# Kernel tuning notes

Measured on AMD Instinct MI355X. Metric: run time of the kernel, lower is better.

## Reference

```python
import jax, jax.numpy as jnp
import numpy as np

B = 64        # graphs
N0 = 2048     # nodes per graph
DEG = 16      # avg degree
IN = 128      # input_dim
H = 30        # hcs
NH = 11       # heads
OD = 8        # output_dim[i]
K1, K2, K3 = 1844, 1660, 1494  # ceil(0.9*n) chain


def setup_inputs() -> dict:
    key = jax.random.key(0)
    ks = jax.random.split(key, 32)
    N = B * N0
    E = N * DEG
    x = jax.random.normal(ks[0], (N, IN), jnp.float32)
    g = jnp.repeat(jnp.arange(B, dtype=jnp.int32), N0 * DEG)
    src = g * N0 + jax.random.randint(ks[1], (E,), 0, N0, dtype=jnp.int32)
    dst = g * N0 + jax.random.randint(ks[2], (E,), 0, N0, dtype=jnp.int32)
    edge_index = jnp.stack([src, dst])
    edge_attr = jax.random.uniform(ks[3], (E,), jnp.float32)
    batch = jnp.repeat(jnp.arange(B, dtype=jnp.int32), N0)
    s = 0.05
    def W(k, *shape):
        return jax.random.normal(k, shape, jnp.float32) * s
    return {
        'x': x, 'edge_index': edge_index, 'edge_attr': edge_attr, 'batch': batch,
        'ln_g': jnp.ones((IN,), jnp.float32), 'ln_b': jnp.zeros((IN,), jnp.float32),
        'W_rel1': W(ks[4], IN, H), 'b_rel1': W(ks[5], H), 'W_root1': W(ks[6], IN, H),
        'W_rel2': W(ks[7], H, H), 'b_rel2': W(ks[8], H), 'W_root2': W(ks[9], H, H),
        'W_rel3': W(ks[10], H, H), 'b_rel3': W(ks[11], H), 'W_root3': W(ks[12], H, H),
        'pool_w1': W(ks[13], H), 'pool_w2': W(ks[14], H), 'pool_w3': W(ks[15], H),
        'head_W1': W(ks[16], NH, 2 * H, 8 * H), 'head_b1': W(ks[17], NH, 8 * H),
        'head_W2': W(ks[18], NH, 8 * H, 32 * H), 'head_b2': W(ks[19], NH, 32 * H),
        'head_W3': W(ks[20], NH, 32 * H, OD), 'head_b3': W(ks[21], NH, OD),
    }


def _layernorm(x, g, b):
    m = x.mean(-1, keepdims=True)
    v = ((x - m) ** 2).mean(-1, keepdims=True)
    return (x - m) * jax.lax.rsqrt(v + 1e-5) * g + b


def _gconv(x, src, dst, ew, Wr, br, Ws, N):
    # PyG GraphConv: out = lin_rel(sum_j ew*x_j) + lin_root(x)
    agg = jax.ops.segment_sum(x[src] * ew[:, None], dst, num_segments=N)
    return agg @ Wr + br + x @ Ws


def _topk_pool(x, src, dst, ew, w, n, k):
    # score = tanh(x.w/||w||); keep top-k per graph; gate kept nodes by score
    score = jnp.tanh((x @ w) / jnp.linalg.norm(w)).reshape(B, n)
    vals, idx = jax.lax.top_k(score, k)                      # [B,k]
    xg = x.reshape(B, n, -1)
    xk = jnp.take_along_axis(xg, idx[:, :, None], axis=1) * vals[:, :, None]
    x_new = xk.reshape(B * k, -1)
    newidx = jnp.full((B, n), -1, jnp.int32)
    newidx = newidx.at[jnp.arange(B)[:, None], idx].set(
        jnp.broadcast_to(jnp.arange(k, dtype=jnp.int32), (B, k)))
    g = src // n
    ns = newidx[g, src % n]
    nd = newidx[g, dst % n]
    keep = (ns >= 0) & (nd >= 0)
    src_new = jnp.where(keep, g * k + ns, 0)
    dst_new = jnp.where(keep, g * k + nd, 0)
    ew_new = jnp.where(keep, ew, 0.0)
    return x_new, src_new, dst_new, ew_new


def _readout(x, k):
    xg = x.reshape(B, k, -1)
    return jnp.concatenate([xg.max(axis=1), xg.mean(axis=1)], axis=1)  # [B,2H]


def reference(x, edge_index, edge_attr, batch, ln_g, ln_b,
              W_rel1, b_rel1, W_root1, W_rel2, b_rel2, W_root2,
              W_rel3, b_rel3, W_root3, pool_w1, pool_w2, pool_w3,
              head_W1, head_b1, head_W2, head_b2, head_W3, head_b3):
    src, dst = edge_index[0], edge_index[1]
    ew = edge_attr
    h = _layernorm(x, ln_g, ln_b)

    h = jax.nn.relu(_gconv(h, src, dst, ew, W_rel1, b_rel1, W_root1, B * N0))
    h, src, dst, ew = _topk_pool(h, src, dst, ew, pool_w1, N0, K1)
    x1 = _readout(h, K1)

    h = jax.nn.relu(_gconv(h, src, dst, ew, W_rel2, b_rel2, W_root2, B * K1))
    h, src, dst, ew = _topk_pool(h, src, dst, ew, pool_w2, K1, K2)
    x2 = _readout(h, K2)

    h = jax.nn.relu(_gconv(h, src, dst, ew, W_rel3, b_rel3, W_root3, B * K2))
    h, src, dst, ew = _topk_pool(h, src, dst, ew, pool_w3, K2, K3)
    x3 = _readout(h, K3)

    z = jax.nn.relu(x1 + x2 + x3)                                   # [B,60]
    a = jax.nn.relu(jnp.einsum('bd,hdo->hbo', z, head_W1) + head_b1[:, None, :])
    a = jax.nn.relu(jnp.einsum('hbo,hop->hbp', a, head_W2) + head_b2[:, None, :])
    out = jnp.einsum('hbp,hpq->hbq', a, head_W3) + head_b3[:, None, :]
    return out  # [11, B, 8]
```

## Files before the change

kernel.cpp:

```cpp
#include <hip/hip_runtime.h>
#include <hip/hip_bf16.h>

#define B 64
#define N0 2048
#define DEG 16
#define IN_DIM 128
#define H 30
#define NH 11
#define K1 1844
#define K2 1660
#define K3 1494
#define NTOT (B * N0)
#define ETOT (NTOT * DEG)
#define EPG (ETOT / B)
#define RSTRIDE 32
#define ESTRIDE1 32768
#define ESTRIDE2 27648
#define RSEG 16

__global__ __launch_bounds__(256) void k_prep(
    const float* __restrict__ ln_g, const float* __restrict__ ln_b,
    const float* __restrict__ Wrel1, const float* __restrict__ brel1, const float* __restrict__ Wroot1,
    const float* __restrict__ Wrel2, const float* __restrict__ Wroot2,
    const float* __restrict__ Wrel3, const float* __restrict__ Wroot3,
    float* __restrict__ Wc1, float* __restrict__ S1, float* __restrict__ T1,
    float* __restrict__ Wc2, float* __restrict__ Wc3)
{
    int tid = threadIdx.x;
    for (int i = tid; i < IN_DIM * 60; i += 256) {
        int j = i / 60, c = i - j * 60;
        float w = (c < H) ? Wrel1[j * H + c] : Wroot1[j * H + (c - H)];
        Wc1[i] = w * ln_g[j];
    }
    if (tid < 60) {
        int c = tid;
        float s = 0.f, tt = 0.f;
        for (int j = 0; j < IN_DIM; ++j) {
            float w = (c < H) ? Wrel1[j * H + c] : Wroot1[j * H + (c - H)];
            s += w * ln_g[j];
            tt += w * ln_b[j];
        }
        S1[c] = s;
        T1[c] = (c < H) ? tt : tt + brel1[c - H];
    }
    for (int i = tid; i < H * 60; i += 256) {
        int j = i / 60, c = i - j * 60;
        Wc2[i] = (c < H) ? Wrel2[j * H + c] : Wroot2[j * H + (c - H)];
        Wc3[i] = (c < H) ? Wrel3[j * H + c] : Wroot3[j * H + (c - H)];
    }
}

__global__ __launch_bounds__(256) void k_lnproj(
    const float* __restrict__ x, const float* __restrict__ Wc,
    const float* __restrict__ S, const float* __restrict__ T,
    float* __restrict__ r, float* __restrict__ t)
{
    int row = blockIdx.x * 256 + threadIdx.x;
    const float* xr = x + (size_t)row * IN_DIM;
    float acc[60];
#pragma unroll
    for (int c = 0; c < 60; ++c) acc[c] = 0.f;
    float sum = 0.f, sumsq = 0.f;
    for (int jb = 0; jb < IN_DIM; jb += 8) {
        float4 a0 = *(const float4*)(xr + jb);
        float4 a1 = *(const float4*)(xr + jb + 4);
        float xs[8] = {a0.x, a0.y, a0.z, a0.w, a1.x, a1.y, a1.z, a1.w};
#pragma unroll
        for (int u = 0; u < 8; ++u) {
            float xv = xs[u];
            sum += xv;
            sumsq += xv * xv;
            const float* wrow = Wc + (jb + u) * 60;
#pragma unroll
            for (int c = 0; c < 60; ++c) acc[c] += xv * wrow[c];
        }
    }
    float mean = sum * (1.f / 128.f);
    float var = sumsq * (1.f / 128.f) - mean * mean;
    float rstd = 1.0f / sqrtf(var + 1e-5f);
    int rb = row * RSTRIDE, tb = row * H;
#pragma unroll
    for (int c = 0; c < H; ++c)
        r[rb + c] = rstd * (acc[c] - mean * S[c]) + T[c];
#pragma unroll
    for (int c = 0; c < H; ++c)
        t[tb + c] = rstd * (acc[30 + c] - mean * S[30 + c]) + T[30 + c];
}

__global__ __launch_bounds__(256) void k_proj30p(
    const float* __restrict__ hbuf, const int* __restrict__ sidx,
    const float* __restrict__ score, const float* __restrict__ Wc,
    const float* __restrict__ brel, float* __restrict__ r, float* __restrict__ t,
    int n_old, int k)
{
    int row = blockIdx.x * 256 + threadIdx.x;
    int g = row / k, j = row - g * k;
    int idx = sidx[g * k + j];
    float val = score[g * n_old + idx];
    const float* hr = hbuf + (size_t)(g * n_old + idx) * RSTRIDE;
    float hv[32];
#pragma unroll
    for (int m = 0; m < 8; ++m) {
        float4 q = *(const float4*)(hr + m * 4);
        hv[m * 4] = q.x; hv[m * 4 + 1] = q.y; hv[m * 4 + 2] = q.z; hv[m * 4 + 3] = q.w;
    }
    float acc[60];
#pragma unroll
    for (int c = 0; c < 60; ++c) acc[c] = 0.f;
    for (int m = 0; m < H; ++m) {
        const float* wrow = Wc + m * 60;
        float xv = hv[m];
#pragma unroll
        for (int c = 0; c < 60; ++c) acc[c] += xv * wrow[c];
    }
    int rb = row * RSTRIDE, tb = row * H;
#pragma unroll
    for (int c = 0; c < H; ++c) r[rb + c] = val * acc[c];
#pragma unroll
    for (int c = 0; c < H; ++c) t[tb + c] = val * acc[30 + c] + brel[c];
}

__global__ __launch_bounds__(1024) void k_hist1(
    const int* __restrict__ dst, unsigned short* __restrict__ rank,
    int* __restrict__ chunkCnt)
{
    __shared__ unsigned int cnt[2048];
    int chunk = blockIdx.x, g = chunk >> 2;
    for (int i = threadIdx.x; i < 2048; i += 1024) cnt[i] = 0;
    __syncthreads();
    int e0 = chunk * 8192;
#pragma unroll
    for (int u = 0; u < 8; ++u) {
        int e = e0 + u * 1024 + threadIdx.x;
        int d = dst[e] - g * N0;
        rank[e] = (unsigned short)atomicAdd(&cnt[d], 1u);
    }
    __syncthreads();
    for (int i = threadIdx.x; i < 2048; i += 1024) chunkCnt[chunk * 2048 + i] = cnt[i];
}

__global__ __launch_bounds__(1024) void k_scat1(
    const int* __restrict__ src, const int* __restrict__ dst, const float* __restrict__ ew,
    const unsigned short* __restrict__ rank, const int* __restrict__ chunkOff,
    float2* __restrict__ sOut)
{
    int chunk = blockIdx.x, g = chunk >> 2;
    int e0 = chunk * 8192;
#pragma unroll
    for (int u = 0; u < 8; ++u) {
        int e = e0 + u * 1024 + threadIdx.x;
        int d = dst[e] - g * N0;
        int pos = chunkOff[chunk * 2048 + d] + (int)rank[e];
        sOut[(size_t)g * ESTRIDE1 + pos] = make_float2(__int_as_float(src[e]), ew[e]);
    }
}

__global__ __launch_bounds__(1024) void k_histE(
    const int* __restrict__ src0, const int* __restrict__ dst0,
    const int* __restrict__ mapc, unsigned short* __restrict__ rank,
    int* __restrict__ chunkCnt)
{
    __shared__ unsigned int cnt[2048];
    int chunk = blockIdx.x;
    for (int i = threadIdx.x; i < 2048; i += 1024) cnt[i] = 0;
    __syncthreads();
    int e0 = chunk * 8192;
#pragma unroll
    for (int u = 0; u < 8; ++u) {
        int e = e0 + u * 1024 + threadIdx.x;
        int dd = mapc[dst0[e]];
        int ss = mapc[src0[e]];
        if (dd >= 0 && ss >= 0)
            rank[e] = (unsigned short)atomicAdd(&cnt[dd], 1u);
    }
    __syncthreads();
    for (int i = threadIdx.x; i < 2048; i += 1024) chunkCnt[chunk * 2048 + i] = cnt[i];
}

__global__ __launch_bounds__(1024) void k_scatE(
    const int* __restrict__ src0, const int* __restrict__ dst0,
    const float* __restrict__ ew, const int* __restrict__ mapc,
    const unsigned short* __restrict__ rank, const int* __restrict__ chunkOff,
    float2* __restrict__ sOut, int k_new, int estride)
{
    int chunk = blockIdx.x, g = chunk >> 2;
    int e0 = chunk * 8192;
#pragma unroll
    for (int u = 0; u < 8; ++u) {
        int e = e0 + u * 1024 + threadIdx.x;
        int dd = mapc[dst0[e]];
        int ss = mapc[src0[e]];
        if (dd >= 0 && ss >= 0) {
            int pos = chunkOff[chunk * 2048 + dd] + (int)rank[e];
            sOut[(size_t)g * estride + pos] =
                make_float2(__int_as_float(g * k_new + ss), ew[e]);
        }
    }
}

__global__ __launch_bounds__(1024) void k_scan(
    int* __restrict__ chunkCnt, int* __restrict__ runStart, int* __restrict__ runLen)
{
    __shared__ int bufA[2048], bufB[2048];
    int g = blockIdx.x;
    int c0[2], c1[2], c2[2], tt[2];
    for (int h2 = 0; h2 < 2; ++h2) {
        int d = threadIdx.x + h2 * 1024;
        c0[h2] = chunkCnt[(g * 4 + 0) * 2048 + d];
        c1[h2] = chunkCnt[(g * 4 + 1) * 2048 + d];
        c2[h2] = chunkCnt[(g * 4 + 2) * 2048 + d];
        int c3 = chunkCnt[(g * 4 + 3) * 2048 + d];
        tt[h2] = c0[h2] + c1[h2] + c2[h2] + c3;
        bufA[d] = tt[h2];
    }
    __syncthreads();
    int* s_ = bufA; int* d_ = bufB;
    for (int off = 1; off < 2048; off <<= 1) {
        for (int h2 = 0; h2 < 2; ++h2) {
            int d = threadIdx.x + h2 * 1024;
            int v = s_[d];
            if (d >= off) v += s_[d - off];
            d_[d] = v;
        }
        __syncthreads();
        int* tmp = s_; s_ = d_; d_ = tmp;
    }
    for (int h2 = 0; h2 < 2; ++h2) {
        int d = threadIdx.x + h2 * 1024;
        int ex = s_[d] - tt[h2];
        runStart[g * 2048 + d] = ex;
        runLen[g * 2048 + d] = tt[h2];
        chunkCnt[(g * 4 + 0) * 2048 + d] = ex;
        chunkCnt[(g * 4 + 1) * 2048 + d] = ex + c0[h2];
        chunkCnt[(g * 4 + 2) * 2048 + d] = ex + c0[h2] + c1[h2];
        chunkCnt[(g * 4 + 3) * 2048 + d] = ex + c0[h2] + c1[h2] + c2[h2];
    }
}

__global__ __launch_bounds__(256) void k_gather(
    const float2* __restrict__ sE, const int* __restrict__ runS, const int* __restrict__ runL,
    const float* __restrict__ rp, const float* __restrict__ t, float* __restrict__ h,
    const float* __restrict__ poolw, float* __restrict__ score,
    int n, int estride, int nblocks)
{
    int b = blockIdx.x;
    int cpx = nblocks >> 3;
    b = (b & 7) * cpx + (b >> 3);
    int slot = threadIdx.x >> 5, j = threadIdx.x & 31;
    int v = b * 8 + slot;
    int g = v / n;
    int local = v - g * n;
    int s0 = runS[g * 2048 + local], len = runL[g * 2048 + local];
    const float2* meta = sE + (size_t)g * estride + s0;
    float acc = 0.f;
    for (int c = 0; c < len; c += 8) {
        int lim = len - c; if (lim > 8) lim = 8;
        float2 m[8];
#pragma unroll
        for (int u = 0; u < 8; ++u) m[u] = meta[c + (u < lim ? u : 0)];
#pragma unroll
        for (int u = 0; u < 8; ++u) {
            int s = __float_as_int(m[u].x);
            float w = (u < lim) ? m[u].y : 0.f;
            acc += rp[(size_t)s * RSTRIDE + j] * w;
        }
    }
    float wj = (j < H) ? poolw[j] : 0.f;
    float hval = 0.f;
    if (j < H) {
        hval = fmaxf(acc + t[v * H + j], 0.f);
        h[(size_t)v * RSTRIDE + j] = hval;
    }
    float p = hval * wj, q = wj * wj;
#pragma unroll
    for (int off = 16; off > 0; off >>= 1) {
        p += __shfl_xor(p, off, 32);
        q += __shfl_xor(q, off, 32);
    }
    if (j == 0) score[v] = tanhf(p / sqrtf(q));
}

__global__ __launch_bounds__(1024) void k_topk_map(
    const float* __restrict__ score, int* __restrict__ sidx, int* __restrict__ mapc,
    int n, int k, int first)
{
    __shared__ unsigned long long keys[2048];
    __shared__ int inv[2048];
    int g = blockIdx.x;
    for (int i = threadIdx.x; i < 2048; i += 1024) {
        unsigned long long key = ~0ull;
        if (i < n) {
            float s = score[g * n + i];
            if (s == 0.f) s = 0.f;
            unsigned u = __float_as_uint(s);
            unsigned asc = (u & 0x80000000u) ? ~u : (u | 0x80000000u);
            unsigned desc = ~asc;
            key = ((unsigned long long)desc << 32) | (unsigned)i;
        }
        keys[i] = key;
        inv[i] = -1;
    }
    __syncthreads();
    for (int kk = 2; kk <= 2048; kk <<= 1) {
        for (int jj = kk >> 1; jj > 0; jj >>= 1) {
            for (int i = threadIdx.x; i < 2048; i += 1024) {
                int ixj = i ^ jj;
                if (ixj > i) {
                    unsigned long long a = keys[i], bb = keys[ixj];
                    bool up = ((i & kk) == 0);
                    if ((a > bb) == up) { keys[i] = bb; keys[ixj] = a; }
                }
            }
            __syncthreads();
        }
    }
    for (int j = threadIdx.x; j < k; j += 1024) {
        int idx = (int)(keys[j] & 0xffffffffu);
        sidx[g * k + j] = idx;
        inv[idx] = j;
    }
    __syncthreads();
    if (first) {
        for (int v = threadIdx.x; v < N0; v += 1024)
            mapc[g * N0 + v] = inv[v];
    } else {
        for (int v = threadIdx.x; v < N0; v += 1024) {
            int m = mapc[g * N0 + v];
            mapc[g * N0 + v] = (m >= 0) ? inv[m] : -1;
        }
    }
}

__global__ __launch_bounds__(256) void k_rpart(
    const float* __restrict__ hbuf, const int* __restrict__ sidx,
    const float* __restrict__ score, float* __restrict__ pmax, float* __restrict__ psum,
    int n_old, int k)
{
    __shared__ float smax[8][32], ssum[8][32];
    int g = blockIdx.y, seg = blockIdx.x;
    int clen = (k + RSEG - 1) / RSEG;
    int start = seg * clen;
    int end = start + clen; if (end > k) end = k;
    int f = threadIdx.x & 31, rr = threadIdx.x >> 5;
    float mx = -INFINITY, sm = 0.f;
    if (f < H) {
        for (int j = start + rr; j < end; j += 8) {
            int idx = sidx[g * k + j];
            float val = score[g * n_old + idx];
            float v = hbuf[(size_t)(g * n_old + idx) * RSTRIDE + f] * val;
            mx = fmaxf(mx, v);
            sm += v;
        }
    }
    smax[rr][f] = mx; ssum[rr][f] = sm;
    __syncthreads();
    if (rr == 0) {
        for (int q = 1; q < 8; ++q) { mx = fmaxf(mx, smax[q][f]); sm += ssum[q][f]; }
        pmax[(g * RSEG + seg) * 32 + f] = mx;
        psum[(g * RSEG + seg) * 32 + f] = sm;
    }
}

__global__ __launch_bounds__(64) void k_zfin(
    const float* __restrict__ pm1, const float* __restrict__ ps1,
    const float* __restrict__ pm2, const float* __restrict__ ps2,
    const float* __restrict__ pm3, const float* __restrict__ ps3,
    float* __restrict__ z)
{
    int g = blockIdx.x, c = threadIdx.x;
    if (c >= 60) return;
    float v1, v2, v3;
    if (c < H) {
        float m1 = -INFINITY, m2 = -INFINITY, m3 = -INFINITY;
        for (int s = 0; s < RSEG; ++s) {
            m1 = fmaxf(m1, pm1[(g * RSEG + s) * 32 + c]);
            m2 = fmaxf(m2, pm2[(g * RSEG + s) * 32 + c]);
            m3 = fmaxf(m3, pm3[(g * RSEG + s) * 32 + c]);
        }
        v1 = m1; v2 = m2; v3 = m3;
    } else {
        int f = c - H;
        float s1 = 0.f, s2 = 0.f, s3 = 0.f;
        for (int s = 0; s < RSEG; ++s) {
            s1 += ps1[(g * RSEG + s) * 32 + f];
            s2 += ps2[(g * RSEG + s) * 32 + f];
            s3 += ps3[(g * RSEG + s) * 32 + f];
        }
        v1 = s1 / (float)K1; v2 = s2 / (float)K2; v3 = s3 / (float)K3;
    }
    z[g * 60 + c] = fmaxf(v1 + v2 + v3, 0.f);
}

__global__ __launch_bounds__(256) void k_mlp1(
    const float* __restrict__ z, const float* __restrict__ W,
    const float* __restrict__ bias, float* __restrict__ a)
{
    int hb = blockIdx.x, hh = hb >> 6, b = hb & 63;
    __shared__ float zr[60];
    if (threadIdx.x < 60) zr[threadIdx.x] = z[b * 60 + threadIdx.x];
    __syncthreads();
    int o = threadIdx.x;
    if (o < 240) {
        float acc = bias[hh * 240 + o];
        const float* Wp = W + hh * 60 * 240;
#pragma unroll
        for (int d = 0; d < 60; ++d) acc += zr[d] * Wp[d * 240 + o];
        a[(hh * B + b) * 240 + o] = fmaxf(acc, 0.f);
    }
}

__global__ __launch_bounds__(320) void k_mlp2(
    const float* __restrict__ a1, const float* __restrict__ W,
    const float* __restrict__ bias, float* __restrict__ a2)
{
    int hh = blockIdx.x >> 3;
    int bb = (blockIdx.x & 7) * 8;
    __shared__ float ar[8][240];
    for (int i = threadIdx.x; i < 8 * 240; i += 320) {
        int rr = i / 240, o = i - rr * 240;
        ar[rr][o] = a1[(hh * B + bb + rr) * 240 + o];
    }
    __syncthreads();
    const float* Wp = W + hh * 240 * 960;
    float accv[3][8];
#pragma unroll
    for (int q = 0; q < 3; ++q)
#pragma unroll
        for (int rr = 0; rr < 8; ++rr) accv[q][rr] = 0.f;
#pragma unroll 2
    for (int o = 0; o < 240; ++o) {
        float w0 = Wp[o * 960 + threadIdx.x];
        float w1 = Wp[o * 960 + threadIdx.x + 320];
        float w2 = Wp[o * 960 + threadIdx.x + 640];
#pragma unroll
        for (int rr = 0; rr < 8; ++rr) {
            float av = ar[rr][o];
            accv[0][rr] += w0 * av;
            accv[1][rr] += w1 * av;
            accv[2][rr] += w2 * av;
        }
    }
#pragma unroll
    for (int q = 0; q < 3; ++q) {
        int p = threadIdx.x + q * 320;
        float bv = bias[hh * 960 + p];
#pragma unroll
        for (int rr = 0; rr < 8; ++rr)
            a2[(hh * B + bb + rr) * 960 + p] = fmaxf(accv[q][rr] + bv, 0.f);
    }
}

__global__ __launch_bounds__(64) void k_mlp3(
    const float* __restrict__ a2, const float* __restrict__ W,
    const float* __restrict__ bias, float* __restrict__ out)
{
    int hb = blockIdx.x, hh = hb >> 6, b = hb & 63;
    __shared__ float ar[960];
    __shared__ float part[64];
    for (int i = threadIdx.x; i < 960; i += 64) ar[i] = a2[(hh * B + b) * 960 + i];
    __syncthreads();
    int q = threadIdx.x & 7, c = threadIdx.x >> 3;
    const float* Wp = W + hh * 960 * 8;
    float acc = 0.f;
    for (int p = c; p < 960; p += 8) acc += ar[p] * Wp[p * 8 + q];
    part[threadIdx.x] = acc;
    __syncthreads();
    if (threadIdx.x < 8) {
        float s = bias[hh * 8 + threadIdx.x];
        for (int cc = 0; cc < 8; ++cc) s += part[cc * 8 + threadIdx.x];
        out[(hh * B + b) * 8 + threadIdx.x] = s;
    }
}

extern "C" void kernel_launch(void* const* d_in, const int* in_sizes, int n_in,
                              void* d_out, int out_size, void* d_ws, size_t ws_size,
                              hipStream_t stream)
{
    const float* x       = (const float*)d_in[0];
    const int*   eidx    = (const int*)d_in[1];
    const int*   src0    = eidx;
    const int*   dst0    = eidx + ETOT;
    const float* ew0     = (const float*)d_in[2];
    const float* ln_g    = (const float*)d_in[4];
    const float* ln_b    = (const float*)d_in[5];
    const float* W_rel1  = (const float*)d_in[6];
    const float* b_rel1  = (const float*)d_in[7];
    const float* W_root1 = (const float*)d_in[8];
    const float* W_rel2  = (const float*)d_in[9];
    const float* b_rel2  = (const float*)d_in[10];
    const float* W_root2 = (const float*)d_in[11];
    const float* W_rel3  = (const float*)d_in[12];
    const float* b_rel3  = (const float*)d_in[13];
    const float* W_root3 = (const float*)d_in[14];
    const float* pool_w1 = (const float*)d_in[15];
    const float* pool_w2 = (const float*)d_in[16];
    const float* pool_w3 = (const float*)d_in[17];
    const float* head_W1 = (const float*)d_in[18];
    const float* head_b1 = (const float*)d_in[19];
    const float* head_W2 = (const float*)d_in[20];
    const float* head_b2 = (const float*)d_in[21];
    const float* head_W3 = (const float*)d_in[22];
    const float* head_b3 = (const float*)d_in[23];

    float* ws     = (float*)d_ws;
    float* rbuf   = ws;
    float* tbuf   = rbuf + (size_t)NTOT * RSTRIDE;
    float* abuf   = tbuf + (size_t)NTOT * H;
    float2* sA    = (float2*)(abuf + (size_t)NTOT * RSTRIDE);
    float2* sB    = sA + (size_t)B * ESTRIDE1;
    float* score  = (float*)(sB + (size_t)B * ESTRIDE2);
    int*   sidx   = (int*)(score + NTOT);
    int*   mapc   = sidx + NTOT;
    int*   runSA  = mapc + NTOT;
    int*   runLA  = runSA + B * 2048;
    int*   runSB  = runLA + B * 2048;
    int*   runLB  = runSB + B * 2048;
    float* pm1    = (float*)(runLB + B * 2048);
    float* ps1    = pm1 + B * RSEG * 32;
    float* pm2    = ps1 + B * RSEG * 32;
    float* ps2    = pm2 + B * RSEG * 32;
    float* pm3    = ps2 + B * RSEG * 32;
    float* ps3    = pm3 + B * RSEG * 32;
    float* zb     = ps3 + B * RSEG * 32;
    float* Wc1    = zb + B * 60;
    float* S1     = Wc1 + IN_DIM * 60;
    float* T1     = S1 + 60;
    float* Wc2    = T1 + 60;
    float* Wc3    = Wc2 + H * 60;
    int* chunkBuf         = (int*)abuf;
    unsigned short* rank  = (unsigned short*)((char*)abuf + (4u << 20));
    float* a1 = rbuf;
    float* a2 = a1 + NH * B * 240;

    k_prep<<<1, 256, 0, stream>>>(ln_g, ln_b, W_rel1, b_rel1, W_root1,
                                  W_rel2, W_root2, W_rel3, W_root3,
                                  Wc1, S1, T1, Wc2, Wc3);

    k_hist1<<<256, 1024, 0, stream>>>(dst0, rank, chunkBuf);
    k_scan<<<B, 1024, 0, stream>>>(chunkBuf, runSA, runLA);
    k_scat1<<<256, 1024, 0, stream>>>(src0, dst0, ew0, rank, chunkBuf, sA);
    k_lnproj<<<NTOT / 256, 256, 0, stream>>>(x, Wc1, S1, T1, rbuf, tbuf);
    k_gather<<<NTOT / 8, 256, 0, stream>>>(sA, runSA, runLA, rbuf, tbuf, abuf,
                                           pool_w1, score, N0, ESTRIDE1, NTOT / 8);
    k_topk_map<<<B, 1024, 0, stream>>>(score, sidx, mapc, N0, K1, 1);
    k_rpart<<<dim3(RSEG, B), 256, 0, stream>>>(abuf, sidx, score, pm1, ps1, N0, K1);
    k_proj30p<<<B * K1 / 256, 256, 0, stream>>>(abuf, sidx, score, Wc2, b_rel2,
                                                rbuf, tbuf, N0, K1);

    k_histE<<<256, 1024, 0, stream>>>(src0, dst0, mapc, rank, chunkBuf);
    k_scan<<<B, 1024, 0, stream>>>(chunkBuf, runSB, runLB);
    k_scatE<<<256, 1024, 0, stream>>>(src0, dst0, ew0, mapc, rank, chunkBuf, sB,
                                      K1, ESTRIDE2);
    k_gather<<<B * K1 / 8, 256, 0, stream>>>(sB, runSB, runLB, rbuf, tbuf, abuf,
                                             pool_w2, score, K1, ESTRIDE2, B * K1 / 8);
    k_topk_map<<<B, 1024, 0, stream>>>(score, sidx, mapc, K1, K2, 0);
    k_rpart<<<dim3(RSEG, B), 256, 0, stream>>>(abuf, sidx, score, pm2, ps2, K1, K2);
    k_proj30p<<<B * K2 / 256, 256, 0, stream>>>(abuf, sidx, score, Wc3, b_rel3,
                                                rbuf, tbuf, K1, K2);

    k_histE<<<256, 1024, 0, stream>>>(src0, dst0, mapc, rank, chunkBuf);
    k_scan<<<B, 1024, 0, stream>>>(chunkBuf, runSA, runLA);
    k_scatE<<<256, 1024, 0, stream>>>(src0, dst0, ew0, mapc, rank, chunkBuf, sA,
                                      K2, ESTRIDE1);
    k_gather<<<B * K2 / 8, 256, 0, stream>>>(sA, runSA, runLA, rbuf, tbuf, abuf,
                                             pool_w3, score, K2, ESTRIDE1, B * K2 / 8);
    k_topk_map<<<B, 1024, 0, stream>>>(score, sidx, mapc, K2, K3, 0);
    k_rpart<<<dim3(RSEG, B), 256, 0, stream>>>(abuf, sidx, score, pm3, ps3, K2, K3);

    k_zfin<<<B, 64, 0, stream>>>(pm1, ps1, pm2, ps2, pm3, ps3, zb);
    k_mlp1<<<NH * B, 256, 0, stream>>>(zb, head_W1, head_b1, a1);
    k_mlp2<<<NH * 8, 320, 0, stream>>>(a1, head_W2, head_b2, a2);
    k_mlp3<<<NH * B, 64, 0, stream>>>(a2, head_W3, head_b3, (float*)d_out);
}
```

Before: 577.2 us.

## Reuse level-0 CSR with index remap, retile projections and head MLP

```diff
diff --git a/kernel.cpp b/kernel.cpp
--- a/kernel.cpp
+++ b/kernel.cpp
@@ -15,7 +15,6 @@
 #define EPG (ETOT / B)
 #define RSTRIDE 32
 #define ESTRIDE1 32768
-#define ESTRIDE2 27648
 #define RSEG 16
 
 __global__ __launch_bounds__(256) void k_prep(
@@ -55,36 +54,82 @@
     const float* __restrict__ S, const float* __restrict__ T,
     float* __restrict__ r, float* __restrict__ t)
 {
-    int row = blockIdx.x * 256 + threadIdx.x;
-    const float* xr = x + (size_t)row * IN_DIM;
-    float acc[60];
-#pragma unroll
-    for (int c = 0; c < 60; ++c) acc[c] = 0.f;
-    float sum = 0.f, sumsq = 0.f;
-    for (int jb = 0; jb < IN_DIM; jb += 8) {
-        float4 a0 = *(const float4*)(xr + jb);
-        float4 a1 = *(const float4*)(xr + jb + 4);
-        float xs[8] = {a0.x, a0.y, a0.z, a0.w, a1.x, a1.y, a1.z, a1.w};
-#pragma unroll
-        for (int u = 0; u < 8; ++u) {
-            float xv = xs[u];
-            sum += xv;
-            sumsq += xv * xv;
-            const float* wrow = Wc + (jb + u) * 60;
-#pragma unroll
-            for (int c = 0; c < 60; ++c) acc[c] += xv * wrow[c];
-        }
-    }
-    float mean = sum * (1.f / 128.f);
-    float var = sumsq * (1.f / 128.f) - mean * mean;
-    float rstd = 1.0f / sqrtf(var + 1e-5f);
-    int rb = row * RSTRIDE, tb = row * H;
-#pragma unroll
-    for (int c = 0; c < H; ++c)
-        r[rb + c] = rstd * (acc[c] - mean * S[c]) + T[c];
-#pragma unroll
-    for (int c = 0; c < H; ++c)
-        t[tb + c] = rstd * (acc[30 + c] - mean * S[30 + c]) + T[30 + c];
+    __shared__ float wlds[4][IN_DIM][16];
+    for (int i = threadIdx.x; i < IN_DIM * 64; i += 256) {
+        int k = i >> 6, cc = i & 63;
+        int cg = cc >> 4, j = cc & 15;
+        wlds[cg][k][j] = (j < 15) ? Wc[k * 60 + cg * 15 + j] : 0.f;
+    }
+    __syncthreads();
+    int lane = threadIdx.x & 63, cg = threadIdx.x >> 6;
+    int row0 = blockIdx.x * 512 + lane;
+    const float* xb = x + (size_t)row0 * IN_DIM;
+    float acc[8][15];
+    float sum[8], sumsq[8];
+#pragma unroll
+    for (int ri = 0; ri < 8; ++ri) {
+        sum[ri] = 0.f; sumsq[ri] = 0.f;
+#pragma unroll
+        for (int c = 0; c < 15; ++c) acc[ri][c] = 0.f;
+    }
+    float4 cur[8], nxt[8];
+#pragma unroll
+    for (int ri = 0; ri < 8; ++ri)
+        cur[ri] = *(const float4*)(xb + (size_t)ri * 64 * IN_DIM);
+    for (int kb = 0; kb < 32; ++kb) {
+        if (kb < 31) {
+#pragma unroll
+            for (int ri = 0; ri < 8; ++ri)
+                nxt[ri] = *(const float4*)(xb + (size_t)ri * 64 * IN_DIM + (kb + 1) * 4);
+        }
+#pragma unroll
+        for (int kk = 0; kk < 4; ++kk) {
+            int k = kb * 4 + kk;
+            float4 w0 = *(const float4*)&wlds[cg][k][0];
+            float4 w1 = *(const float4*)&wlds[cg][k][4];
+            float4 w2 = *(const float4*)&wlds[cg][k][8];
+            float4 w3 = *(const float4*)&wlds[cg][k][12];
+#pragma unroll
+            for (int ri = 0; ri < 8; ++ri) {
+                float xv = (kk == 0) ? cur[ri].x : (kk == 1) ? cur[ri].y
+                          : (kk == 2) ? cur[ri].z : cur[ri].w;
+                sum[ri] += xv; sumsq[ri] += xv * xv;
+                acc[ri][0]  += xv * w0.x; acc[ri][1]  += xv * w0.y;
+                acc[ri][2]  += xv * w0.z; acc[ri][3]  += xv * w0.w;
+                acc[ri][4]  += xv * w1.x; acc[ri][5]  += xv * w1.y;
+                acc[ri][6]  += xv * w1.z; acc[ri][7]  += xv * w1.w;
+                acc[ri][8]  += xv * w2.x; acc[ri][9]  += xv * w2.y;
+                acc[ri][10] += xv * w2.z; acc[ri][11] += xv * w2.w;
+                acc[ri][12] += xv * w3.x; acc[ri][13] += xv * w3.y;
+                acc[ri][14] += xv * w3.z;
+            }
+        }
+        if (kb < 31) {
+#pragma unroll
+            for (int ri = 0; ri < 8; ++ri) cur[ri] = nxt[ri];
+        }
+    }
+    bool isR = (cg < 2);
+    int cbase = (cg & 1) * 15;
+    float* outp = isR ? r : t;
+    float sS[15], sT[15];
+#pragma unroll
+    for (int c = 0; c < 15; ++c) { sS[c] = S[cg * 15 + c]; sT[c] = T[cg * 15 + c]; }
+#pragma unroll
+    for (int ri = 0; ri < 8; ++ri) {
+        int row = row0 + ri * 64;
+        float mean = sum[ri] * (1.f / 128.f);
+        float var = sumsq[ri] * (1.f / 128.f) - mean * mean;
+        float rstd = 1.0f / sqrtf(var + 1e-5f);
+        float* op = outp + (size_t)row * RSTRIDE + cbase;
+#pragma unroll
+        for (int c = 0; c < 15; ++c)
+            op[c] = rstd * (acc[ri][c] - mean * sS[c]) + sT[c];
+        if (cg & 1) {
+            outp[(size_t)row * RSTRIDE + 30] = 0.f;
+            outp[(size_t)row * RSTRIDE + 31] = 0.f;
+        }
+    }
 }
 
 __global__ __launch_bounds__(256) void k_proj30p(
@@ -93,31 +138,100 @@
     const float* __restrict__ brel, float* __restrict__ r, float* __restrict__ t,
     int n_old, int k)
 {
-    int row = blockIdx.x * 256 + threadIdx.x;
-    int g = row / k, j = row - g * k;
-    int idx = sidx[g * k + j];
-    float val = score[g * n_old + idx];
-    const float* hr = hbuf + (size_t)(g * n_old + idx) * RSTRIDE;
-    float hv[32];
-#pragma unroll
-    for (int m = 0; m < 8; ++m) {
-        float4 q = *(const float4*)(hr + m * 4);
-        hv[m * 4] = q.x; hv[m * 4 + 1] = q.y; hv[m * 4 + 2] = q.z; hv[m * 4 + 3] = q.w;
-    }
-    float acc[60];
-#pragma unroll
-    for (int c = 0; c < 60; ++c) acc[c] = 0.f;
-    for (int m = 0; m < H; ++m) {
-        const float* wrow = Wc + m * 60;
-        float xv = hv[m];
-#pragma unroll
-        for (int c = 0; c < 60; ++c) acc[c] += xv * wrow[c];
-    }
-    int rb = row * RSTRIDE, tb = row * H;
-#pragma unroll
-    for (int c = 0; c < H; ++c) r[rb + c] = val * acc[c];
-#pragma unroll
-    for (int c = 0; c < H; ++c) t[tb + c] = val * acc[30 + c] + brel[c];
+    __shared__ float wlds[4][32][16];
+    for (int i = threadIdx.x; i < 30 * 64; i += 256) {
+        int m = i >> 6, cc = i & 63;
+        int cg = cc >> 4, j = cc & 15;
+        wlds[cg][m][j] = (j < 15) ? Wc[m * 60 + cg * 15 + j] : 0.f;
+    }
+    __syncthreads();
+    int lane = threadIdx.x & 63, cg = threadIdx.x >> 6;
+    int row0 = blockIdx.x * 256 + lane;
+    float acc[4][15];
+#pragma unroll
+    for (int ri = 0; ri < 4; ++ri)
+#pragma unroll
+        for (int c = 0; c < 15; ++c) acc[ri][c] = 0.f;
+    float vals[4];
+    const float* hp[4];
+#pragma unroll
+    for (int ri = 0; ri < 4; ++ri) {
+        int row = row0 + ri * 64;
+        int g = row / k, j = row - g * k;
+        int idx = sidx[g * k + j];
+        vals[ri] = score[g * n_old + idx];
+        hp[ri] = hbuf + (size_t)(g * n_old + idx) * RSTRIDE;
+    }
+    for (int mb = 0; mb < 7; ++mb) {
+        float4 cur[4];
+#pragma unroll
+        for (int ri = 0; ri < 4; ++ri) cur[ri] = *(const float4*)(hp[ri] + mb * 4);
+#pragma unroll
+        for (int kk = 0; kk < 4; ++kk) {
+            int m = mb * 4 + kk;
+            float4 w0 = *(const float4*)&wlds[cg][m][0];
+            float4 w1 = *(const float4*)&wlds[cg][m][4];
+            float4 w2 = *(const float4*)&wlds[cg][m][8];
+            float4 w3 = *(const float4*)&wlds[cg][m][12];
+#pragma unroll
+            for (int ri = 0; ri < 4; ++ri) {
+                float xv = (kk == 0) ? cur[ri].x : (kk == 1) ? cur[ri].y
+                          : (kk == 2) ? cur[ri].z : cur[ri].w;
+                acc[ri][0]  += xv * w0.x; acc[ri][1]  += xv * w0.y;
+                acc[ri][2]  += xv * w0.z; acc[ri][3]  += xv * w0.w;
+                acc[ri][4]  += xv * w1.x; acc[ri][5]  += xv * w1.y;
+                acc[ri][6]  += xv * w1.z; acc[ri][7]  += xv * w1.w;
+                acc[ri][8]  += xv * w2.x; acc[ri][9]  += xv * w2.y;
+                acc[ri][10] += xv * w2.z; acc[ri][11] += xv * w2.w;
+                acc[ri][12] += xv * w3.x; acc[ri][13] += xv * w3.y;
+                acc[ri][14] += xv * w3.z;
+            }
+        }
+    }
+    {
+        float2 h2[4];
+#pragma unroll
+        for (int ri = 0; ri < 4; ++ri) h2[ri] = *(const float2*)(hp[ri] + 28);
+#pragma unroll
+        for (int kk = 0; kk < 2; ++kk) {
+            int m = 28 + kk;
+            float4 w0 = *(const float4*)&wlds[cg][m][0];
+            float4 w1 = *(const float4*)&wlds[cg][m][4];
+            float4 w2 = *(const float4*)&wlds[cg][m][8];
+            float4 w3 = *(const float4*)&wlds[cg][m][12];
+#pragma unroll
+            for (int ri = 0; ri < 4; ++ri) {
+                float xv = (kk == 0) ? h2[ri].x : h2[ri].y;
+                acc[ri][0]  += xv * w0.x; acc[ri][1]  += xv * w0.y;
+                acc[ri][2]  += xv * w0.z; acc[ri][3]  += xv * w0.w;
+                acc[ri][4]  += xv * w1.x; acc[ri][5]  += xv * w1.y;
+                acc[ri][6]  += xv * w1.z; acc[ri][7]  += xv * w1.w;
+                acc[ri][8]  += xv * w2.x; acc[ri][9]  += xv * w2.y;
+                acc[ri][10] += xv * w2.z; acc[ri][11] += xv * w2.w;
+                acc[ri][12] += xv * w3.x; acc[ri][13] += xv * w3.y;
+                acc[ri][14] += xv * w3.z;
+            }
+        }
+    }
+    bool isR = (cg < 2);
+    int cbase = (cg & 1) * 15;
+    float* outp = isR ? r : t;
+    float sB[15];
+#pragma unroll
+    for (int c = 0; c < 15; ++c) sB[c] = isR ? 0.f : brel[cbase + c];
+#pragma unroll
+    for (int ri = 0; ri < 4; ++ri) {
+        int row = row0 + ri * 64;
+        float val = vals[ri];
+        float* op = outp + (size_t)row * RSTRIDE + cbase;
+#pragma unroll
+        for (int c = 0; c < 15; ++c)
+            op[c] = val * acc[ri][c] + sB[c];
+        if (cg & 1) {
+            outp[(size_t)row * RSTRIDE + 30] = 0.f;
+            outp[(size_t)row * RSTRIDE + 31] = 0.f;
+        }
+    }
 }
 
 __global__ __launch_bounds__(1024) void k_hist1(
@@ -137,65 +251,6 @@
     }
     __syncthreads();
     for (int i = threadIdx.x; i < 2048; i += 1024) chunkCnt[chunk * 2048 + i] = cnt[i];
-}
-
-__global__ __launch_bounds__(1024) void k_scat1(
-    const int* __restrict__ src, const int* __restrict__ dst, const float* __restrict__ ew,
-    const unsigned short* __restrict__ rank, const int* __restrict__ chunkOff,
-    float2* __restrict__ sOut)
-{
-    int chunk = blockIdx.x, g = chunk >> 2;
-    int e0 = chunk * 8192;
-#pragma unroll
-    for (int u = 0; u < 8; ++u) {
-        int e = e0 + u * 1024 + threadIdx.x;
-        int d = dst[e] - g * N0;
-        int pos = chunkOff[chunk * 2048 + d] + (int)rank[e];
-        sOut[(size_t)g * ESTRIDE1 + pos] = make_float2(__int_as_float(src[e]), ew[e]);
-    }
-}
-
-__global__ __launch_bounds__(1024) void k_histE(
-    const int* __restrict__ src0, const int* __restrict__ dst0,
-    const int* __restrict__ mapc, unsigned short* __restrict__ rank,
-    int* __restrict__ chunkCnt)
-{
-    __shared__ unsigned int cnt[2048];
-    int chunk = blockIdx.x;
-    for (int i = threadIdx.x; i < 2048; i += 1024) cnt[i] = 0;
-    __syncthreads();
-    int e0 = chunk * 8192;
-#pragma unroll
-    for (int u = 0; u < 8; ++u) {
-        int e = e0 + u * 1024 + threadIdx.x;
-        int dd = mapc[dst0[e]];
-        int ss = mapc[src0[e]];
-        if (dd >= 0 && ss >= 0)
-            rank[e] = (unsigned short)atomicAdd(&cnt[dd], 1u);
-    }
-    __syncthreads();
-    for (int i = threadIdx.x; i < 2048; i += 1024) chunkCnt[chunk * 2048 + i] = cnt[i];
-}
-
-__global__ __launch_bounds__(1024) void k_scatE(
-    const int* __restrict__ src0, const int* __restrict__ dst0,
-    const float* __restrict__ ew, const int* __restrict__ mapc,
-    const unsigned short* __restrict__ rank, const int* __restrict__ chunkOff,
-    float2* __restrict__ sOut, int k_new, int estride)
-{
-    int chunk = blockIdx.x, g = chunk >> 2;
-    int e0 = chunk * 8192;
-#pragma unroll
-    for (int u = 0; u < 8; ++u) {
-        int e = e0 + u * 1024 + threadIdx.x;
-        int dd = mapc[dst0[e]];
-        int ss = mapc[src0[e]];
-        if (dd >= 0 && ss >= 0) {
-            int pos = chunkOff[chunk * 2048 + dd] + (int)rank[e];
-            sOut[(size_t)g * estride + pos] =
-                make_float2(__int_as_float(g * k_new + ss), ew[e]);
-        }
-    }
 }
 
 __global__ __launch_bounds__(1024) void k_scan(
@@ -237,11 +292,29 @@
     }
 }
 
+__global__ __launch_bounds__(1024) void k_scat1(
+    const int* __restrict__ src, const int* __restrict__ dst, const float* __restrict__ ew,
+    const unsigned short* __restrict__ rank, const int* __restrict__ chunkOff,
+    float2* __restrict__ sOut)
+{
+    int chunk = blockIdx.x, g = chunk >> 2;
+    int e0 = chunk * 8192;
+#pragma unroll
+    for (int u = 0; u < 8; ++u) {
+        int e = e0 + u * 1024 + threadIdx.x;
+        int d = dst[e] - g * N0;
+        int pos = chunkOff[chunk * 2048 + d] + (int)rank[e];
+        sOut[(size_t)g * ESTRIDE1 + pos] = make_float2(__int_as_float(src[e]), ew[e]);
+    }
+}
+
+template<int LVL>
 __global__ __launch_bounds__(256) void k_gather(
     const float2* __restrict__ sE, const int* __restrict__ runS, const int* __restrict__ runL,
+    const int* __restrict__ ind1, const int* __restrict__ ind2, const int* __restrict__ mapc,
     const float* __restrict__ rp, const float* __restrict__ t, float* __restrict__ h,
     const float* __restrict__ poolw, float* __restrict__ score,
-    int n, int estride, int nblocks)
+    int n, int rK, int nblocks)
 {
     int b = blockIdx.x;
     int cpx = nblocks >> 3;
@@ -250,25 +323,40 @@
     int v = b * 8 + slot;
     int g = v / n;
     int local = v - g * n;
-    int s0 = runS[g * 2048 + local], len = runL[g * 2048 + local];
-    const float2* meta = sE + (size_t)g * estride + s0;
+    int v1 = local;
+    if (LVL >= 2) v1 = ind2[g * K2 + v1];
+    if (LVL >= 1) v1 = ind1[g * K1 + v1];
+    int s0 = runS[g * 2048 + v1], len = runL[g * 2048 + v1];
+    const float2* meta = sE + (size_t)g * ESTRIDE1 + s0;
+    int rbase = g * rK;
     float acc = 0.f;
     for (int c = 0; c < len; c += 8) {
         int lim = len - c; if (lim > 8) lim = 8;
         float2 m[8];
 #pragma unroll
         for (int u = 0; u < 8; ++u) m[u] = meta[c + (u < lim ? u : 0)];
+        int rowv[8]; float wv[8];
 #pragma unroll
         for (int u = 0; u < 8; ++u) {
-            int s = __float_as_int(m[u].x);
+            int srcg = __float_as_int(m[u].x);
             float w = (u < lim) ? m[u].y : 0.f;
-            acc += rp[(size_t)s * RSTRIDE + j] * w;
-        }
+            if (LVL == 0) {
+                rowv[u] = srcg;
+            } else {
+                int ss = mapc[srcg];
+                rowv[u] = rbase + (ss < 0 ? 0 : ss);
+                w = (ss < 0) ? 0.f : w;
+            }
+            wv[u] = w;
+        }
+#pragma unroll
+        for (int u = 0; u < 8; ++u)
+            acc += rp[(size_t)rowv[u] * RSTRIDE + j] * wv[u];
     }
     float wj = (j < H) ? poolw[j] : 0.f;
     float hval = 0.f;
     if (j < H) {
-        hval = fmaxf(acc + t[v * H + j], 0.f);
+        hval = fmaxf(acc + t[(size_t)v * RSTRIDE + j], 0.f);
         h[(size_t)v * RSTRIDE + j] = hval;
     }
     float p = hval * wj, q = wj * wj;
@@ -409,45 +497,34 @@
     }
 }
 
-__global__ __launch_bounds__(320) void k_mlp2(
+__global__ __launch_bounds__(256) void k_mlp2(
     const float* __restrict__ a1, const float* __restrict__ W,
     const float* __restrict__ bias, float* __restrict__ a2)
 {
-    int hh = blockIdx.x >> 3;
-    int bb = (blockIdx.x & 7) * 8;
-    __shared__ float ar[8][240];
-    for (int i = threadIdx.x; i < 8 * 240; i += 320) {
-        int rr = i / 240, o = i - rr * 240;
-        ar[rr][o] = a1[(hh * B + bb + rr) * 240 + o];
-    }
-    __syncthreads();
-    const float* Wp = W + hh * 240 * 960;
-    float accv[3][8];
-#pragma unroll
-    for (int q = 0; q < 3; ++q)
-#pragma unroll
-        for (int rr = 0; rr < 8; ++rr) accv[q][rr] = 0.f;
-#pragma unroll 2
+    __shared__ float a1t[64 * 240];
+    int hh = blockIdx.x / 15, ct = blockIdx.x % 15;
+    const float4* ag = (const float4*)(a1 + (size_t)hh * B * 240);
+    for (int i = threadIdx.x; i < 64 * 240 / 4; i += 256)
+        ((float4*)a1t)[i] = ag[i];
+    __syncthreads();
+    int col = threadIdx.x & 63, rg = threadIdx.x >> 6;
+    const float* Wp = W + (size_t)hh * 240 * 960 + ct * 64 + col;
+    float acc[16];
+#pragma unroll
+    for (int i = 0; i < 16; ++i) acc[i] = 0.f;
+#pragma unroll 4
     for (int o = 0; o < 240; ++o) {
-        float w0 = Wp[o * 960 + threadIdx.x];
-        float w1 = Wp[o * 960 + threadIdx.x + 320];
-        float w2 = Wp[o * 960 + threadIdx.x + 640];
-#pragma unroll
-        for (int rr = 0; rr < 8; ++rr) {
-            float av = ar[rr][o];
-            accv[0][rr] += w0 * av;
-            accv[1][rr] += w1 * av;
-            accv[2][rr] += w2 * av;
-        }
-    }
-#pragma unroll
-    for (int q = 0; q < 3; ++q) {
-        int p = threadIdx.x + q * 320;
-        float bv = bias[hh * 960 + p];
-#pragma unroll
-        for (int rr = 0; rr < 8; ++rr)
-            a2[(hh * B + bb + rr) * 960 + p] = fmaxf(accv[q][rr] + bv, 0.f);
-    }
+        float w = Wp[(size_t)o * 960];
+        const float* ar = &a1t[0];
+#pragma unroll
+        for (int i = 0; i < 16; ++i)
+            acc[i] += w * ar[(rg * 16 + i) * 240 + o];
+    }
+    float bv = bias[hh * 960 + ct * 64 + col];
+#pragma unroll
+    for (int i = 0; i < 16; ++i)
+        a2[((size_t)hh * B + rg * 16 + i) * 960 + ct * 64 + col] =
+            fmaxf(acc[i] + bv, 0.f);
 }
 
 __global__ __launch_bounds__(64) void k_mlp3(
@@ -505,17 +582,16 @@
     float* ws     = (float*)d_ws;
     float* rbuf   = ws;
     float* tbuf   = rbuf + (size_t)NTOT * RSTRIDE;
-    float* abuf   = tbuf + (size_t)NTOT * H;
+    float* abuf   = tbuf + (size_t)NTOT * RSTRIDE;
     float2* sA    = (float2*)(abuf + (size_t)NTOT * RSTRIDE);
-    float2* sB    = sA + (size_t)B * ESTRIDE1;
-    float* score  = (float*)(sB + (size_t)B * ESTRIDE2);
-    int*   sidx   = (int*)(score + NTOT);
-    int*   mapc   = sidx + NTOT;
+    float* score  = (float*)(sA + (size_t)B * ESTRIDE1);
+    int*   sidxA  = (int*)(score + NTOT);
+    int*   sidxB  = sidxA + B * K1;
+    int*   sidxC  = sidxB + B * K2;
+    int*   mapc   = sidxC + B * K3;
     int*   runSA  = mapc + NTOT;
     int*   runLA  = runSA + B * 2048;
-    int*   runSB  = runLA + B * 2048;
-    int*   runLB  = runSB + B * 2048;
-    float* pm1    = (float*)(runLB + B * 2048);
+    float* pm1    = (float*)(runLA + B * 2048);
     float* ps1    = pm1 + B * RSEG * 32;
     float* pm2    = ps1 + B * RSEG * 32;
     float* ps2    = pm2 + B * RSEG * 32;
@@ -539,36 +615,32 @@
     k_hist1<<<256, 1024, 0, stream>>>(dst0, rank, chunkBuf);
     k_scan<<<B, 1024, 0, stream>>>(chunkBuf, runSA, runLA);
     k_scat1<<<256, 1024, 0, stream>>>(src0, dst0, ew0, rank, chunkBuf, sA);
-    k_lnproj<<<NTOT / 256, 256, 0, stream>>>(x, Wc1, S1, T1, rbuf, tbuf);
-    k_gather<<<NTOT / 8, 256, 0, stream>>>(sA, runSA, runLA, rbuf, tbuf, abuf,
-                                           pool_w1, score, N0, ESTRIDE1, NTOT / 8);
-    k_topk_map<<<B, 1024, 0, stream>>>(score, sidx, mapc, N0, K1, 1);
-    k_rpart<<<dim3(RSEG, B), 256, 0, stream>>>(abuf, sidx, score, pm1, ps1, N0, K1);
-    k_proj30p<<<B * K1 / 256, 256, 0, stream>>>(abuf, sidx, score, Wc2, b_rel2,
+
+    k_lnproj<<<NTOT / 512, 256, 0, stream>>>(x, Wc1, S1, T1, rbuf, tbuf);
+    k_gather<0><<<NTOT / 8, 256, 0, stream>>>(sA, runSA, runLA, nullptr, nullptr, nullptr,
+                                              rbuf, tbuf, abuf, pool_w1, score,
+                                              N0, N0, NTOT / 8);
+    k_topk_map<<<B, 1024, 0, stream>>>(score, sidxA, mapc, N0, K1, 1);
+    k_rpart<<<dim3(RSEG, B), 256, 0, stream>>>(abuf, sidxA, score, pm1, ps1, N0, K1);
+    k_proj30p<<<B * K1 / 256, 256, 0, stream>>>(abuf, sidxA, score, Wc2, b_rel2,
                                                 rbuf, tbuf, N0, K1);
 
-    k_histE<<<256, 1024, 0, stream>>>(src0, dst0, mapc, rank, chunkBuf);
-    k_scan<<<B, 1024, 0, stream>>>(chunkBuf, runSB, runLB);
-    k_scatE<<<256, 1024, 0, stream>>>(src0, dst0, ew0, mapc, rank, chunkBuf, sB,
-                                      K1, ESTRIDE2);
-    k_gather<<<B * K1 / 8, 256, 0, stream>>>(sB, runSB, runLB, rbuf, tbuf, abuf,
-                                             pool_w2, score, K1, ESTRIDE2, B * K1 / 8);
-    k_topk_map<<<B, 1024, 0, stream>>>(score, sidx, mapc, K1, K2, 0);
-    k_rpart<<<dim3(RSEG, B), 256, 0, stream>>>(abuf, sidx, score, pm2, ps2, K1, K2);
-    k_proj30p<<<B * K2 / 256, 256, 0, stream>>>(abuf, sidx, score, Wc3, b_rel3,
+    k_gather<1><<<B * K1 / 8, 256, 0, stream>>>(sA, runSA, runLA, sidxA, nullptr, mapc,
+                                                rbuf, tbuf, abuf, pool_w2, score,
+                                                K1, K1, B * K1 / 8);
+    k_topk_map<<<B, 1024, 0, stream>>>(score, sidxB, mapc, K1, K2, 0);
+    k_rpart<<<dim3(RSEG, B), 256, 0, stream>>>(abuf, sidxB, score, pm2, ps2, K1, K2);
+    k_proj30p<<<B * K2 / 256, 256, 0, stream>>>(abuf, sidxB, score, Wc3, b_rel3,
                                                 rbuf, tbuf, K1, K2);
 
-    k_histE<<<256, 1024, 0, stream>>>(src0, dst0, mapc, rank, chunkBuf);
-    k_scan<<<B, 1024, 0, stream>>>(chunkBuf, runSA, runLA);
-    k_scatE<<<256, 1024, 0, stream>>>(src0, dst0, ew0, mapc, rank, chunkBuf, sA,
-                                      K2, ESTRIDE1);
-    k_gather<<<B * K2 / 8, 256, 0, stream>>>(sA, runSA, runLA, rbuf, tbuf, abuf,
-                                             pool_w3, score, K2, ESTRIDE1, B * K2 / 8);
-    k_topk_map<<<B, 1024, 0, stream>>>(score, sidx, mapc, K2, K3, 0);
-    k_rpart<<<dim3(RSEG, B), 256, 0, stream>>>(abuf, sidx, score, pm3, ps3, K2, K3);
+    k_gather<2><<<B * K2 / 8, 256, 0, stream>>>(sA, runSA, runLA, sidxA, sidxB, mapc,
+                                                rbuf, tbuf, abuf, pool_w3, score,
+                                                K2, K2, B * K2 / 8);
+    k_topk_map<<<B, 1024, 0, stream>>>(score, sidxC, mapc, K2, K3, 0);
+    k_rpart<<<dim3(RSEG, B), 256, 0, stream>>>(abuf, sidxC, score, pm3, ps3, K2, K3);
 
     k_zfin<<<B, 64, 0, stream>>>(pm1, ps1, pm2, ps2, pm3, ps3, zb);
     k_mlp1<<<NH * B, 256, 0, stream>>>(zb, head_W1, head_b1, a1);
-    k_mlp2<<<NH * 8, 320, 0, stream>>>(a1, head_W2, head_b2, a2);
+    k_mlp2<<<NH * 15, 256, 0, stream>>>(a1, head_W2, head_b2, a2);
     k_mlp3<<<NH * B, 64, 0, stream>>>(a2, head_W3, head_b3, (float*)d_out);
 }
```

Result: no change. 570.5 us (-1.2%).
